# Performance work log

Hardware: AMD Instinct MI355X
Metric: run time of the kernel (lower is better)

The kernel has to match this reference:

```python
import jax, jax.numpy as jnp
import numpy as np

IN_DIM, HIDDEN_DIM, OUT_DIM = 128, 64, 64
N_NODES, N_EDGES = 100000, 1000000


def gcn_layer(x, src, dst, W, b):
    """PyG GCNConv: h = W x; out = D^-1/2 (A+I) D^-1/2 h + b (self-loops already in src/dst)."""
    n = x.shape[0]
    deg = jax.ops.segment_sum(jnp.ones_like(src, dtype=x.dtype), dst, num_segments=n)
    dinv = jnp.where(deg > 0, jax.lax.rsqrt(deg), 0.0)
    norm = dinv[src] * dinv[dst]          # [E+N]
    h = x @ W                              # [N, out]
    msg = h[src] * norm[:, None]           # [E+N, out] gather + scale
    out = jax.ops.segment_sum(msg, dst, num_segments=n)  # scatter-add
    return out + b


def setup_inputs() -> dict:
    key = jax.random.key(0)
    k1, k2, k3, k4 = jax.random.split(key, 4)
    x = jax.random.normal(k1, (N_NODES, IN_DIM), dtype=jnp.float32)
    edge_index = jax.random.randint(k2, (2, N_EDGES), 0, N_NODES, dtype=jnp.int64)
    # Glorot-ish init for the two GCNConv linear weights; zero biases (PyG default)
    W1 = jax.random.normal(k3, (IN_DIM, HIDDEN_DIM), dtype=jnp.float32) / np.sqrt(IN_DIM)
    W2 = jax.random.normal(k4, (HIDDEN_DIM, OUT_DIM), dtype=jnp.float32) / np.sqrt(HIDDEN_DIM)
    b1 = jnp.zeros((HIDDEN_DIM,), dtype=jnp.float32)
    b2 = jnp.zeros((OUT_DIM,), dtype=jnp.float32)
    return {"x": x, "edge_index": edge_index, "W1": W1, "b1": b1, "W2": W2, "b2": b2}


def reference(x, edge_index, W1, b1, W2, b2):
    n = x.shape[0]
    loops = jnp.arange(n, dtype=edge_index.dtype)
    src = jnp.concatenate([edge_index[0], loops])  # add self-loops once
    dst = jnp.concatenate([edge_index[1], loops])
    x1 = gcn_layer(x, src, dst, W1, b1)
    h = jax.nn.relu(x1)
    # dropout is identity in eval/reference mode
    x2 = gcn_layer(h, src, dst, W2, b2)
    return x2
```

## Files before the change

kernel.cpp:

```cpp
#include <hip/hip_runtime.h>
#include <hip/hip_fp16.h>

#define DIM_IN 128
#define DIM_HID 64
#define BK_SHIFT 9
#define BK_SIZE 512
#define SRC_BITS 17
#define CAP 6144
#define CAP2 8192

typedef _Float16 half8 __attribute__((ext_vector_type(8)));
typedef float floatx4 __attribute__((ext_vector_type(4)));


__global__ void zero_kernel(int* __restrict__ p) { p[threadIdx.x] = 0; }


#define P_EPT  16
#define P_TILE 4096

__global__ __launch_bounds__(256)
void partition_kernel(const int* __restrict__ src, const int* __restrict__ dst,
                      int* __restrict__ bcur, int* __restrict__ part, int E) {
    __shared__ int hist[256];
    __shared__ int bofs[256];
    __shared__ int gbase[256];
    __shared__ int stage[P_TILE];
    __shared__ unsigned char auxb[P_TILE];
    const int tid   = threadIdx.x;
    const int tile0 = blockIdx.x * P_TILE;
    const int tcnt  = min(P_TILE, E - tile0);

    hist[tid] = 0;
    __syncthreads();

    int pack[P_EPT], bb[P_EPT], lo[P_EPT];
#pragma unroll
    for (int i = 0; i < P_EPT; ++i) {
        int e = tile0 + i * 256 + tid;
        bb[i] = -1;
        if (e < E) {
            int d = dst[e];
            int s = src[e];
            bb[i]   = d >> BK_SHIFT;
            pack[i] = ((d & (BK_SIZE - 1)) << SRC_BITS) | s;
            lo[i]   = atomicAdd(&hist[bb[i]], 1);
        }
    }
    __syncthreads();

    bofs[tid] = hist[tid];
    __syncthreads();
    for (int off = 1; off < 256; off <<= 1) {
        int t = (tid >= off) ? bofs[tid - off] : 0;
        __syncthreads();
        bofs[tid] += t;
        __syncthreads();
    }
    int ex = bofs[tid] - hist[tid];
    __syncthreads();
    bofs[tid] = ex;
    if (hist[tid]) gbase[tid] = tid * CAP + atomicAdd(&bcur[tid], hist[tid]);
    __syncthreads();

#pragma unroll
    for (int i = 0; i < P_EPT; ++i) {
        if (bb[i] >= 0) {
            int p = bofs[bb[i]] + lo[i];
            stage[p] = pack[i];
            auxb[p]  = (unsigned char)bb[i];
        }
    }
    __syncthreads();

    for (int k = tid; k < tcnt; k += 256) {
        int b = auxb[k];
        part[gbase[b] + (k - bofs[b])] = stage[k];
    }
}


__global__ __launch_bounds__(256)
void bucket_fill_kernel(const int* __restrict__ bcur, const int* __restrict__ part,
                        int2* __restrict__ nodeinfo, float* __restrict__ dinv,
                        int* __restrict__ srcs, int n, int zrow) {
    __shared__ int cnt[BK_SIZE];
    __shared__ int rp[BK_SIZE];
    __shared__ int s2[256];
    __shared__ int total;
    const int tid   = threadIdx.x;
    const int bid   = blockIdx.x;
    const int node0 = bid << BK_SHIFT;
    const int bs    = min(BK_SIZE, n - node0);
    const int pbase = bid * CAP;
    const int sbase = bid * CAP2;
    const int ecnt  = bcur[bid];

    cnt[tid] = 0; cnt[tid + 256] = 0;
    __syncthreads();
    for (int k = tid; k < ecnt; k += 256)
        atomicAdd(&cnt[part[pbase + k] >> SRC_BITS], 1);
    __syncthreads();

    int c0 = cnt[2 * tid], c1 = cnt[2 * tid + 1];
    int p0 = (c0 + 3) & ~3, p1 = (c1 + 3) & ~3;
    s2[tid] = p0 + p1;
    __syncthreads();
    for (int off = 1; off < 256; off <<= 1) {
        int t = (tid >= off) ? s2[tid - off] : 0;
        __syncthreads();
        s2[tid] += t;
        __syncthreads();
    }
    int ex = s2[tid] - (p0 + p1);
    rp[2 * tid]     = ex;
    rp[2 * tid + 1] = ex + p0;
    if (tid == 255) total = s2[255];
    __syncthreads();

    for (int i = tid; i < bs; i += 256) {
        int c = cnt[i];
        nodeinfo[node0 + i] = make_int2(sbase + rp[i], (c + 3) & ~3);
        dinv[node0 + i]     = rsqrtf((float)c + 1.0f);
    }
    __syncthreads();

    cnt[tid] = 0; cnt[tid + 256] = 0;
    for (int k = tid; k < total; k += 256) srcs[sbase + k] = zrow;
    __syncthreads();
    for (int k = tid; k < ecnt; k += 256) {
        int v    = part[pbase + k];
        int li   = v >> SRC_BITS;
        int slot = atomicAdd(&cnt[li], 1);
        srcs[sbase + rp[li] + slot] = v & ((1 << SRC_BITS) - 1);
    }
}


template <int K, bool RELU, typename T>
__launch_bounds__(256)
__global__ void gemm_mfma_kernel(const T* __restrict__ x, const float* __restrict__ W,
                                 const float* __restrict__ dinv, _Float16* __restrict__ out,
                                 int n) {
    constexpr int LDK = K + 8;
    __shared__ _Float16 Wt[64 * LDK];
    const int tid = threadIdx.x;

    for (int idx = tid; idx < K * 64; idx += 256) {
        int k = idx >> 6, c = idx & 63;
        Wt[c * LDK + k] = (_Float16)W[idx];
    }
    __syncthreads();

    const int wave = tid >> 6;
    const int lane = tid & 63;
    const int r    = lane & 15;
    const int g    = lane >> 4;
    const int row0 = blockIdx.x * 64 + wave * 16;
    const int arow = row0 + r;
    const T* xrow = x + (size_t)(arow < n ? arow : 0) * K + g * 8;

    floatx4 acc0 = {}, acc1 = {}, acc2 = {}, acc3 = {};

#pragma unroll
    for (int kt = 0; kt < K / 32; ++kt) {
        half8 a;
        if constexpr (sizeof(T) == 4) {
            float4 a0 = *(const float4*)(xrow + kt * 32);
            float4 a1 = *(const float4*)(xrow + kt * 32 + 4);
            if (RELU) {
                a0.x = fmaxf(a0.x, 0.f); a0.y = fmaxf(a0.y, 0.f);
                a0.z = fmaxf(a0.z, 0.f); a0.w = fmaxf(a0.w, 0.f);
                a1.x = fmaxf(a1.x, 0.f); a1.y = fmaxf(a1.y, 0.f);
                a1.z = fmaxf(a1.z, 0.f); a1.w = fmaxf(a1.w, 0.f);
            }
            a[0] = (_Float16)a0.x; a[1] = (_Float16)a0.y;
            a[2] = (_Float16)a0.z; a[3] = (_Float16)a0.w;
            a[4] = (_Float16)a1.x; a[5] = (_Float16)a1.y;
            a[6] = (_Float16)a1.z; a[7] = (_Float16)a1.w;
        } else {
            a = *(const half8*)(xrow + kt * 32);
            if (RELU) {
#pragma unroll
                for (int i = 0; i < 8; ++i)
                    a[i] = a[i] > (_Float16)0 ? a[i] : (_Float16)0;
            }
        }

        const _Float16* wb = &Wt[r * LDK + kt * 32 + g * 8];
        half8 b0 = *(const half8*)(wb + 0 * 16 * LDK);
        half8 b1 = *(const half8*)(wb + 1 * 16 * LDK);
        half8 b2 = *(const half8*)(wb + 2 * 16 * LDK);
        half8 b3 = *(const half8*)(wb + 3 * 16 * LDK);
        acc0 = __builtin_amdgcn_mfma_f32_16x16x32_f16(a, b0, acc0, 0, 0, 0);
        acc1 = __builtin_amdgcn_mfma_f32_16x16x32_f16(a, b1, acc1, 0, 0, 0);
        acc2 = __builtin_amdgcn_mfma_f32_16x16x32_f16(a, b2, acc2, 0, 0, 0);
        acc3 = __builtin_amdgcn_mfma_f32_16x16x32_f16(a, b3, acc3, 0, 0, 0);
    }

#pragma unroll
    for (int j = 0; j < 4; ++j) {
        int drow = row0 + g * 4 + j;
        _Float16* o = out + (size_t)drow * 64 + r;
        if (drow < n) {
            float dn = dinv[drow];
            o[0]  = (_Float16)(acc0[j] * dn);
            o[16] = (_Float16)(acc1[j] * dn);
            o[32] = (_Float16)(acc2[j] * dn);
            o[48] = (_Float16)(acc3[j] * dn);
        } else {
            o[0] = (_Float16)0; o[16] = (_Float16)0;
            o[32] = (_Float16)0; o[48] = (_Float16)0;
        }
    }
}


template <typename OUT>
__global__ __launch_bounds__(256)
void gather_kernel(const int2* __restrict__ nodeinfo, const int* __restrict__ srcs,
                   const float* __restrict__ dinv, const half8* __restrict__ hs,
                   const float* __restrict__ b, OUT* __restrict__ out, int n) {
    const int tid  = threadIdx.x;
    const int f    = tid & 7;
    const int node = blockIdx.x * 32 + (tid >> 3);
    if (node >= n) return;

    int2 info = nodeinfo[node];
    int start = info.x, cpad = info.y;

    half8 sv = hs[(size_t)node * 8 + f];
    float acc[8];
#pragma unroll
    for (int i = 0; i < 8; ++i) acc[i] = (float)sv[i];

    for (int j = 0; j < cpad; j += 4) {
        int s0 = srcs[start + j + 0];
        int s1 = srcs[start + j + 1];
        int s2 = srcs[start + j + 2];
        int s3 = srcs[start + j + 3];
        half8 v0 = hs[(size_t)s0 * 8 + f];
        half8 v1 = hs[(size_t)s1 * 8 + f];
        half8 v2 = hs[(size_t)s2 * 8 + f];
        half8 v3 = hs[(size_t)s3 * 8 + f];
#pragma unroll
        for (int i = 0; i < 8; ++i)
            acc[i] += ((float)v0[i] + (float)v1[i]) + ((float)v2[i] + (float)v3[i]);
    }

    float dn = dinv[node];
    if constexpr (sizeof(OUT) == 2) {
        half8 o;
#pragma unroll
        for (int i = 0; i < 8; ++i) o[i] = (_Float16)fmaf(acc[i], dn, b[f * 8 + i]);
        ((half8*)out)[(size_t)node * 8 + f] = o;
    } else {
        const float4* b4 = (const float4*)b;
        float4 bb0 = b4[f * 2], bb1 = b4[f * 2 + 1];
        float4 o0 = make_float4(fmaf(acc[0], dn, bb0.x), fmaf(acc[1], dn, bb0.y),
                                fmaf(acc[2], dn, bb0.z), fmaf(acc[3], dn, bb0.w));
        float4 o1 = make_float4(fmaf(acc[4], dn, bb1.x), fmaf(acc[5], dn, bb1.y),
                                fmaf(acc[6], dn, bb1.z), fmaf(acc[7], dn, bb1.w));
        float4* o4 = (float4*)out;
        o4[(size_t)node * 16 + f * 2]     = o0;
        o4[(size_t)node * 16 + f * 2 + 1] = o1;
    }
}


extern "C" void kernel_launch(void* const* d_in, const int* in_sizes, int n_in,
                              void* d_out, int out_size, void* d_ws, size_t ws_size,
                              hipStream_t stream) {
    const float* x   = (const float*)d_in[0];
    const int*   ei  = (const int*)d_in[1];
    const float* W1  = (const float*)d_in[2];
    const float* b1  = (const float*)d_in[3];
    const float* W2  = (const float*)d_in[4];
    const float* b2  = (const float*)d_in[5];
    float*       out = (float*)d_out;

    const int n = in_sizes[0] / DIM_IN;
    const int E = in_sizes[1] / 2;
    const int* srcp = ei;
    const int* dstp = ei + E;
    const int NB    = (n + BK_SIZE - 1) >> BK_SHIFT;
    const int nrows = ((n + 63) / 64) * 64;

    const int npad = ((n + 255) / 256) * 256;

    int*      bcur     = (int*)d_ws;
    int2*     nodeinfo = (int2*)(bcur + 256);
    float*    dinv     = (float*)((int*)nodeinfo + 2 * npad);
    int*      srcs     = (int*)(dinv + npad);
    _Float16* g1       = (_Float16*)(srcs + (size_t)NB * CAP2);
    _Float16* h        = g1 + (size_t)n * 64;
    int*      part     = (int*)g1;

    const int gb = (n + 63) / 64;
    const int ab = (n + 31) / 32;
    const int pb = (E + P_TILE - 1) / P_TILE;

    zero_kernel<<<1, 256, 0, stream>>>(bcur);
    partition_kernel<<<pb, 256, 0, stream>>>(srcp, dstp, bcur, part, E);
    bucket_fill_kernel<<<NB, 256, 0, stream>>>(bcur, part, nodeinfo, dinv, srcs, n, n);

    gemm_mfma_kernel<DIM_IN, false, float><<<gb, 256, 0, stream>>>(x, W1, dinv, h, n);
    gather_kernel<_Float16><<<ab, 256, 0, stream>>>(nodeinfo, srcs, dinv, (const half8*)h,
                                                    b1, g1, n);

    gemm_mfma_kernel<DIM_HID, true, _Float16><<<gb, 256, 0, stream>>>(g1, W2, dinv, h, n);
    gather_kernel<float><<<ab, 256, 0, stream>>>(nodeinfo, srcs, dinv, (const half8*)h,
                                                 b2, out, n);
}
```

Measured before the change: 111.5 us.

## Fuse GEMM1 with edge partitioning and fuse layer-1 gather with GEMM2

The first GEMM no longer depends on degree normalisation, so it runs in the same launch as the edge partitioning kernel, with blocks split by blockIdx. The source-side dinv scaling moves into the gathers as a per-edge dinv lookup. That lets the layer-1 aggregation, bias, ReLU and the second GEMM be fused into one kernel through LDS, removing the g1 round trip and two launches. In exchange each gathered edge does an extra dinv load, and a sentinel dinv entry for the padding row is zeroed.

Measured after the change: 102.1 us. 1.09x faster.

```diff
diff --git a/kernel.cpp b/kernel.cpp
--- a/kernel.cpp
+++ b/kernel.cpp
@@ -8,74 +8,135 @@
 #define SRC_BITS 17
 #define CAP 6144
 #define CAP2 8192
+#define P_EPT  16
+#define P_TILE 4096
 
 typedef _Float16 half8 __attribute__((ext_vector_type(8)));
 typedef float floatx4 __attribute__((ext_vector_type(4)));
 
 
-__global__ void zero_kernel(int* __restrict__ p) { p[threadIdx.x] = 0; }
-
-
-#define P_EPT  16
-#define P_TILE 4096
+__global__ void zero_kernel(int* __restrict__ bcur, float* __restrict__ dinv_sent) {
+    bcur[threadIdx.x] = 0;
+    if (threadIdx.x == 0) dinv_sent[0] = 0.0f;
+}
+
 
 __global__ __launch_bounds__(256)
-void partition_kernel(const int* __restrict__ src, const int* __restrict__ dst,
-                      int* __restrict__ bcur, int* __restrict__ part, int E) {
-    __shared__ int hist[256];
-    __shared__ int bofs[256];
-    __shared__ int gbase[256];
-    __shared__ int stage[P_TILE];
-    __shared__ unsigned char auxb[P_TILE];
-    const int tid   = threadIdx.x;
-    const int tile0 = blockIdx.x * P_TILE;
-    const int tcnt  = min(P_TILE, E - tile0);
-
-    hist[tid] = 0;
-    __syncthreads();
-
-    int pack[P_EPT], bb[P_EPT], lo[P_EPT];
-#pragma unroll
-    for (int i = 0; i < P_EPT; ++i) {
-        int e = tile0 + i * 256 + tid;
-        bb[i] = -1;
-        if (e < E) {
-            int d = dst[e];
-            int s = src[e];
-            bb[i]   = d >> BK_SHIFT;
-            pack[i] = ((d & (BK_SIZE - 1)) << SRC_BITS) | s;
-            lo[i]   = atomicAdd(&hist[bb[i]], 1);
-        }
-    }
-    __syncthreads();
-
-    bofs[tid] = hist[tid];
-    __syncthreads();
-    for (int off = 1; off < 256; off <<= 1) {
-        int t = (tid >= off) ? bofs[tid - off] : 0;
-        __syncthreads();
-        bofs[tid] += t;
-        __syncthreads();
-    }
-    int ex = bofs[tid] - hist[tid];
-    __syncthreads();
-    bofs[tid] = ex;
-    if (hist[tid]) gbase[tid] = tid * CAP + atomicAdd(&bcur[tid], hist[tid]);
-    __syncthreads();
-
-#pragma unroll
-    for (int i = 0; i < P_EPT; ++i) {
-        if (bb[i] >= 0) {
-            int p = bofs[bb[i]] + lo[i];
-            stage[p] = pack[i];
-            auxb[p]  = (unsigned char)bb[i];
-        }
-    }
-    __syncthreads();
-
-    for (int k = tid; k < tcnt; k += 256) {
-        int b = auxb[k];
-        part[gbase[b] + (k - bofs[b])] = stage[k];
+void gemm1_partition_kernel(const float* __restrict__ x, const float* __restrict__ W,
+                            _Float16* __restrict__ h, int n, int gb,
+                            const int* __restrict__ src, const int* __restrict__ dst,
+                            int* __restrict__ bcur, int* __restrict__ part, int E) {
+    __shared__ int smem[5888];
+    const int tid = threadIdx.x;
+
+    if (blockIdx.x < gb) {
+        constexpr int K = DIM_IN, LDK = K + 8;
+        _Float16* Wt = (_Float16*)smem;
+        for (int idx = tid; idx < K * 64; idx += 256) {
+            int k = idx >> 6, c = idx & 63;
+            Wt[c * LDK + k] = (_Float16)W[idx];
+        }
+        __syncthreads();
+
+        const int wave = tid >> 6;
+        const int lane = tid & 63;
+        const int r    = lane & 15;
+        const int g    = lane >> 4;
+        const int row0 = blockIdx.x * 64 + wave * 16;
+        const int arow = row0 + r;
+        const float* xrow = x + (size_t)(arow < n ? arow : 0) * K + g * 8;
+
+        floatx4 acc0 = {}, acc1 = {}, acc2 = {}, acc3 = {};
+#pragma unroll
+        for (int kt = 0; kt < K / 32; ++kt) {
+            float4 a0 = *(const float4*)(xrow + kt * 32);
+            float4 a1 = *(const float4*)(xrow + kt * 32 + 4);
+            half8 a;
+            a[0] = (_Float16)a0.x; a[1] = (_Float16)a0.y;
+            a[2] = (_Float16)a0.z; a[3] = (_Float16)a0.w;
+            a[4] = (_Float16)a1.x; a[5] = (_Float16)a1.y;
+            a[6] = (_Float16)a1.z; a[7] = (_Float16)a1.w;
+
+            const _Float16* wb = &Wt[r * LDK + kt * 32 + g * 8];
+            half8 b0 = *(const half8*)(wb + 0 * 16 * LDK);
+            half8 b1 = *(const half8*)(wb + 1 * 16 * LDK);
+            half8 b2 = *(const half8*)(wb + 2 * 16 * LDK);
+            half8 b3 = *(const half8*)(wb + 3 * 16 * LDK);
+            acc0 = __builtin_amdgcn_mfma_f32_16x16x32_f16(a, b0, acc0, 0, 0, 0);
+            acc1 = __builtin_amdgcn_mfma_f32_16x16x32_f16(a, b1, acc1, 0, 0, 0);
+            acc2 = __builtin_amdgcn_mfma_f32_16x16x32_f16(a, b2, acc2, 0, 0, 0);
+            acc3 = __builtin_amdgcn_mfma_f32_16x16x32_f16(a, b3, acc3, 0, 0, 0);
+        }
+
+#pragma unroll
+        for (int j = 0; j < 4; ++j) {
+            int drow = row0 + g * 4 + j;
+            _Float16* o = h + (size_t)drow * 64 + r;
+            if (drow < n) {
+                o[0]  = (_Float16)acc0[j];
+                o[16] = (_Float16)acc1[j];
+                o[32] = (_Float16)acc2[j];
+                o[48] = (_Float16)acc3[j];
+            } else {
+                o[0] = (_Float16)0; o[16] = (_Float16)0;
+                o[32] = (_Float16)0; o[48] = (_Float16)0;
+            }
+        }
+    } else {
+        int* hist  = smem;
+        int* bofs  = smem + 256;
+        int* gbase = smem + 512;
+        int* stage = smem + 768;
+        unsigned char* auxb = (unsigned char*)(smem + 4864);
+        const int tile0 = (blockIdx.x - gb) * P_TILE;
+        const int tcnt  = min(P_TILE, E - tile0);
+
+        hist[tid] = 0;
+        __syncthreads();
+
+        int pack[P_EPT], bb[P_EPT], lo[P_EPT];
+#pragma unroll
+        for (int i = 0; i < P_EPT; ++i) {
+            int e = tile0 + i * 256 + tid;
+            bb[i] = -1;
+            if (e < E) {
+                int d = dst[e];
+                int s = src[e];
+                bb[i]   = d >> BK_SHIFT;
+                pack[i] = ((d & (BK_SIZE - 1)) << SRC_BITS) | s;
+                lo[i]   = atomicAdd(&hist[bb[i]], 1);
+            }
+        }
+        __syncthreads();
+
+        bofs[tid] = hist[tid];
+        __syncthreads();
+        for (int off = 1; off < 256; off <<= 1) {
+            int t = (tid >= off) ? bofs[tid - off] : 0;
+            __syncthreads();
+            bofs[tid] += t;
+            __syncthreads();
+        }
+        int ex = bofs[tid] - hist[tid];
+        __syncthreads();
+        bofs[tid] = ex;
+        if (hist[tid]) gbase[tid] = tid * CAP + atomicAdd(&bcur[tid], hist[tid]);
+        __syncthreads();
+
+#pragma unroll
+        for (int i = 0; i < P_EPT; ++i) {
+            if (bb[i] >= 0) {
+                int p = bofs[bb[i]] + lo[i];
+                stage[p] = pack[i];
+                auxb[p]  = (unsigned char)bb[i];
+            }
+        }
+        __syncthreads();
+
+        for (int k = tid; k < tcnt; k += 256) {
+            int b = auxb[k];
+            part[gbase[b] + (k - bofs[b])] = stage[k];
+        }
     }
 }
 
@@ -137,18 +198,57 @@
 }
 
 
-template <int K, bool RELU, typename T>
-__launch_bounds__(256)
-__global__ void gemm_mfma_kernel(const T* __restrict__ x, const float* __restrict__ W,
-                                 const float* __restrict__ dinv, _Float16* __restrict__ out,
-                                 int n) {
-    constexpr int LDK = K + 8;
-    __shared__ _Float16 Wt[64 * LDK];
+__global__ __launch_bounds__(256)
+void layer2_fused_kernel(const int2* __restrict__ nodeinfo, const int* __restrict__ srcs,
+                         const float* __restrict__ dinv, const half8* __restrict__ hs,
+                         const float* __restrict__ b1, const float* __restrict__ W2,
+                         _Float16* __restrict__ h2, int n) {
+    __shared__ _Float16 At[64 * 72];
+    __shared__ _Float16 Wt[64 * 72];
     const int tid = threadIdx.x;
 
-    for (int idx = tid; idx < K * 64; idx += 256) {
+    for (int idx = tid; idx < 64 * 64; idx += 256) {
         int k = idx >> 6, c = idx & 63;
-        Wt[c * LDK + k] = (_Float16)W[idx];
+        Wt[c * 72 + k] = (_Float16)W2[idx];
+    }
+
+    const int f    = tid & 7;
+    const int grp  = tid >> 3;
+    const int row0 = blockIdx.x * 64;
+
+#pragma unroll
+    for (int rnd = 0; rnd < 2; ++rnd) {
+        const int nrow = rnd * 32 + grp;
+        const int node = row0 + nrow;
+        half8 o = {};
+        if (node < n) {
+            int2 info = nodeinfo[node];
+            int start = info.x, cpad = info.y;
+            float dn = dinv[node];
+            half8 sv = hs[(size_t)node * 8 + f];
+            float acc[8];
+#pragma unroll
+            for (int i = 0; i < 8; ++i) acc[i] = dn * (float)sv[i];
+
+            for (int j = 0; j < cpad; j += 4) {
+                int4 ss = *(const int4*)&srcs[start + j];
+                float d0 = dinv[ss.x], d1 = dinv[ss.y], d2 = dinv[ss.z], d3 = dinv[ss.w];
+                half8 v0 = hs[(size_t)ss.x * 8 + f];
+                half8 v1 = hs[(size_t)ss.y * 8 + f];
+                half8 v2 = hs[(size_t)ss.z * 8 + f];
+                half8 v3 = hs[(size_t)ss.w * 8 + f];
+#pragma unroll
+                for (int i = 0; i < 8; ++i)
+                    acc[i] += (d0 * (float)v0[i] + d1 * (float)v1[i]) +
+                              (d2 * (float)v2[i] + d3 * (float)v3[i]);
+            }
+#pragma unroll
+            for (int i = 0; i < 8; ++i) {
+                float g1 = fmaf(acc[i], dn, b1[f * 8 + i]);
+                o[i] = (_Float16)fmaxf(g1, 0.0f);
+            }
+        }
+        *(half8*)&At[nrow * 72 + f * 8] = o;
     }
     __syncthreads();
 
@@ -156,71 +256,38 @@
     const int lane = tid & 63;
     const int r    = lane & 15;
     const int g    = lane >> 4;
-    const int row0 = blockIdx.x * 64 + wave * 16;
-    const int arow = row0 + r;
-    const T* xrow = x + (size_t)(arow < n ? arow : 0) * K + g * 8;
 
     floatx4 acc0 = {}, acc1 = {}, acc2 = {}, acc3 = {};
-
-#pragma unroll
-    for (int kt = 0; kt < K / 32; ++kt) {
-        half8 a;
-        if constexpr (sizeof(T) == 4) {
-            float4 a0 = *(const float4*)(xrow + kt * 32);
-            float4 a1 = *(const float4*)(xrow + kt * 32 + 4);
-            if (RELU) {
-                a0.x = fmaxf(a0.x, 0.f); a0.y = fmaxf(a0.y, 0.f);
-                a0.z = fmaxf(a0.z, 0.f); a0.w = fmaxf(a0.w, 0.f);
-                a1.x = fmaxf(a1.x, 0.f); a1.y = fmaxf(a1.y, 0.f);
-                a1.z = fmaxf(a1.z, 0.f); a1.w = fmaxf(a1.w, 0.f);
-            }
-            a[0] = (_Float16)a0.x; a[1] = (_Float16)a0.y;
-            a[2] = (_Float16)a0.z; a[3] = (_Float16)a0.w;
-            a[4] = (_Float16)a1.x; a[5] = (_Float16)a1.y;
-            a[6] = (_Float16)a1.z; a[7] = (_Float16)a1.w;
-        } else {
-            a = *(const half8*)(xrow + kt * 32);
-            if (RELU) {
-#pragma unroll
-                for (int i = 0; i < 8; ++i)
-                    a[i] = a[i] > (_Float16)0 ? a[i] : (_Float16)0;
-            }
-        }
-
-        const _Float16* wb = &Wt[r * LDK + kt * 32 + g * 8];
-        half8 b0 = *(const half8*)(wb + 0 * 16 * LDK);
-        half8 b1 = *(const half8*)(wb + 1 * 16 * LDK);
-        half8 b2 = *(const half8*)(wb + 2 * 16 * LDK);
-        half8 b3 = *(const half8*)(wb + 3 * 16 * LDK);
+#pragma unroll
+    for (int kt = 0; kt < 2; ++kt) {
+        half8 a = *(const half8*)&At[(wave * 16 + r) * 72 + kt * 32 + g * 8];
+        const _Float16* wb = &Wt[r * 72 + kt * 32 + g * 8];
+        half8 b0 = *(const half8*)(wb + 0 * 16 * 72);
+        half8 b1v = *(const half8*)(wb + 1 * 16 * 72);
+        half8 b2v = *(const half8*)(wb + 2 * 16 * 72);
+        half8 b3v = *(const half8*)(wb + 3 * 16 * 72);
         acc0 = __builtin_amdgcn_mfma_f32_16x16x32_f16(a, b0, acc0, 0, 0, 0);
-        acc1 = __builtin_amdgcn_mfma_f32_16x16x32_f16(a, b1, acc1, 0, 0, 0);
-        acc2 = __builtin_amdgcn_mfma_f32_16x16x32_f16(a, b2, acc2, 0, 0, 0);
-        acc3 = __builtin_amdgcn_mfma_f32_16x16x32_f16(a, b3, acc3, 0, 0, 0);
+        acc1 = __builtin_amdgcn_mfma_f32_16x16x32_f16(a, b1v, acc1, 0, 0, 0);
+        acc2 = __builtin_amdgcn_mfma_f32_16x16x32_f16(a, b2v, acc2, 0, 0, 0);
+        acc3 = __builtin_amdgcn_mfma_f32_16x16x32_f16(a, b3v, acc3, 0, 0, 0);
     }
 
 #pragma unroll
     for (int j = 0; j < 4; ++j) {
-        int drow = row0 + g * 4 + j;
-        _Float16* o = out + (size_t)drow * 64 + r;
-        if (drow < n) {
-            float dn = dinv[drow];
-            o[0]  = (_Float16)(acc0[j] * dn);
-            o[16] = (_Float16)(acc1[j] * dn);
-            o[32] = (_Float16)(acc2[j] * dn);
-            o[48] = (_Float16)(acc3[j] * dn);
-        } else {
-            o[0] = (_Float16)0; o[16] = (_Float16)0;
-            o[32] = (_Float16)0; o[48] = (_Float16)0;
-        }
-    }
-}
-
-
-template <typename OUT>
+        int drow = row0 + wave * 16 + g * 4 + j;
+        _Float16* o = h2 + (size_t)drow * 64 + r;
+        o[0]  = (_Float16)acc0[j];
+        o[16] = (_Float16)acc1[j];
+        o[32] = (_Float16)acc2[j];
+        o[48] = (_Float16)acc3[j];
+    }
+}
+
+
 __global__ __launch_bounds__(256)
-void gather_kernel(const int2* __restrict__ nodeinfo, const int* __restrict__ srcs,
-                   const float* __restrict__ dinv, const half8* __restrict__ hs,
-                   const float* __restrict__ b, OUT* __restrict__ out, int n) {
+void gather_out_kernel(const int2* __restrict__ nodeinfo, const int* __restrict__ srcs,
+                       const float* __restrict__ dinv, const half8* __restrict__ hs,
+                       const float* __restrict__ b, float* __restrict__ out, int n) {
     const int tid  = threadIdx.x;
     const int f    = tid & 7;
     const int node = blockIdx.x * 32 + (tid >> 3);
@@ -228,43 +295,35 @@
 
     int2 info = nodeinfo[node];
     int start = info.x, cpad = info.y;
+    float dn = dinv[node];
 
     half8 sv = hs[(size_t)node * 8 + f];
     float acc[8];
 #pragma unroll
-    for (int i = 0; i < 8; ++i) acc[i] = (float)sv[i];
+    for (int i = 0; i < 8; ++i) acc[i] = dn * (float)sv[i];
 
     for (int j = 0; j < cpad; j += 4) {
-        int s0 = srcs[start + j + 0];
-        int s1 = srcs[start + j + 1];
-        int s2 = srcs[start + j + 2];
-        int s3 = srcs[start + j + 3];
-        half8 v0 = hs[(size_t)s0 * 8 + f];
-        half8 v1 = hs[(size_t)s1 * 8 + f];
-        half8 v2 = hs[(size_t)s2 * 8 + f];
-        half8 v3 = hs[(size_t)s3 * 8 + f];
+        int4 ss = *(const int4*)&srcs[start + j];
+        float d0 = dinv[ss.x], d1 = dinv[ss.y], d2 = dinv[ss.z], d3 = dinv[ss.w];
+        half8 v0 = hs[(size_t)ss.x * 8 + f];
+        half8 v1 = hs[(size_t)ss.y * 8 + f];
+        half8 v2 = hs[(size_t)ss.z * 8 + f];
+        half8 v3 = hs[(size_t)ss.w * 8 + f];
 #pragma unroll
         for (int i = 0; i < 8; ++i)
-            acc[i] += ((float)v0[i] + (float)v1[i]) + ((float)v2[i] + (float)v3[i]);
-    }
-
-    float dn = dinv[node];
-    if constexpr (sizeof(OUT) == 2) {
-        half8 o;
-#pragma unroll
-        for (int i = 0; i < 8; ++i) o[i] = (_Float16)fmaf(acc[i], dn, b[f * 8 + i]);
-        ((half8*)out)[(size_t)node * 8 + f] = o;
-    } else {
-        const float4* b4 = (const float4*)b;
-        float4 bb0 = b4[f * 2], bb1 = b4[f * 2 + 1];
-        float4 o0 = make_float4(fmaf(acc[0], dn, bb0.x), fmaf(acc[1], dn, bb0.y),
-                                fmaf(acc[2], dn, bb0.z), fmaf(acc[3], dn, bb0.w));
-        float4 o1 = make_float4(fmaf(acc[4], dn, bb1.x), fmaf(acc[5], dn, bb1.y),
-                                fmaf(acc[6], dn, bb1.z), fmaf(acc[7], dn, bb1.w));
-        float4* o4 = (float4*)out;
-        o4[(size_t)node * 16 + f * 2]     = o0;
-        o4[(size_t)node * 16 + f * 2 + 1] = o1;
-    }
+            acc[i] += (d0 * (float)v0[i] + d1 * (float)v1[i]) +
+                      (d2 * (float)v2[i] + d3 * (float)v3[i]);
+    }
+
+    const float4* b4 = (const float4*)b;
+    float4 bb0 = b4[f * 2], bb1 = b4[f * 2 + 1];
+    float4 o0 = make_float4(fmaf(acc[0], dn, bb0.x), fmaf(acc[1], dn, bb0.y),
+                            fmaf(acc[2], dn, bb0.z), fmaf(acc[3], dn, bb0.w));
+    float4 o1 = make_float4(fmaf(acc[4], dn, bb1.x), fmaf(acc[5], dn, bb1.y),
+                            fmaf(acc[6], dn, bb1.z), fmaf(acc[7], dn, bb1.w));
+    float4* o4 = (float4*)out;
+    o4[(size_t)node * 16 + f * 2]     = o0;
+    o4[(size_t)node * 16 + f * 2 + 1] = o1;
 }
 
 
@@ -284,7 +343,10 @@
     const int* srcp = ei;
     const int* dstp = ei + E;
     const int NB    = (n + BK_SIZE - 1) >> BK_SHIFT;
-    const int nrows = ((n + 63) / 64) * 64;
+    const int gb    = (n + 63) / 64;
+    const int pb    = (E + P_TILE - 1) / P_TILE;
+    const int ab    = (n + 31) / 32;
+    const size_t nrows = (size_t)gb * 64;
 
     const int npad = ((n + 255) / 256) * 256;
 
@@ -292,23 +354,16 @@
     int2*     nodeinfo = (int2*)(bcur + 256);
     float*    dinv     = (float*)((int*)nodeinfo + 2 * npad);
     int*      srcs     = (int*)(dinv + npad);
-    _Float16* g1       = (_Float16*)(srcs + (size_t)NB * CAP2);
-    _Float16* h        = g1 + (size_t)n * 64;
-    int*      part     = (int*)g1;
-
-    const int gb = (n + 63) / 64;
-    const int ab = (n + 31) / 32;
-    const int pb = (E + P_TILE - 1) / P_TILE;
-
-    zero_kernel<<<1, 256, 0, stream>>>(bcur);
-    partition_kernel<<<pb, 256, 0, stream>>>(srcp, dstp, bcur, part, E);
+    int*      part     = srcs + (size_t)NB * CAP2;
+    _Float16* h        = (_Float16*)(part + (size_t)NB * CAP);
+    _Float16* h2       = h + nrows * 64;
+
+    zero_kernel<<<1, 256, 0, stream>>>(bcur, &dinv[n]);
+    gemm1_partition_kernel<<<gb + pb, 256, 0, stream>>>(x, W1, h, n, gb,
+                                                        srcp, dstp, bcur, part, E);
     bucket_fill_kernel<<<NB, 256, 0, stream>>>(bcur, part, nodeinfo, dinv, srcs, n, n);
-
-    gemm_mfma_kernel<DIM_IN, false, float><<<gb, 256, 0, stream>>>(x, W1, dinv, h, n);
-    gather_kernel<_Float16><<<ab, 256, 0, stream>>>(nodeinfo, srcs, dinv, (const half8*)h,
-                                                    b1, g1, n);
-
-    gemm_mfma_kernel<DIM_HID, true, _Float16><<<gb, 256, 0, stream>>>(g1, W2, dinv, h, n);
-    gather_kernel<float><<<ab, 256, 0, stream>>>(nodeinfo, srcs, dinv, (const half8*)h,
-                                                 b2, out, n);
-}
+    layer2_fused_kernel<<<gb, 256, 0, stream>>>(nodeinfo, srcs, dinv, (const half8*)h,
+                                                b1, W2, h2, n);
+    gather_out_kernel<<<ab, 256, 0, stream>>>(nodeinfo, srcs, dinv, (const half8*)h2,
+                                              b2, out, n);
+}
```
